# Optimization experiments

Measured on AMD Instinct MI355X. Metric: run time of the kernel, lower is better.

Reference implementation:

```python
import jax, jax.numpy as jnp
import numpy as np

B, S = 64, 128
NQ, C = 2000, 128
K, DE, DC = 64, 64, 64


def _glorot(k, shape):
    lim = float(np.sqrt(6.0 / (shape[0] + shape[1])))
    return jax.random.uniform(k, shape, jnp.float32, -lim, lim)


def setup_inputs() -> dict:
    key = jax.random.key(0)
    ks = jax.random.split(key, 16)
    return {
        'question_seq': jax.random.randint(ks[0], (B, S), 0, NQ, dtype=jnp.int32),
        'correctness_seq': jax.random.randint(ks[1], (B, S), 0, 2, dtype=jnp.int32),
        'q_matrix': (jax.random.uniform(ks[2], (NQ, C)) < 0.15).astype(jnp.float32),
        'E_q': jax.random.normal(ks[3], (NQ, DE), jnp.float32) * 0.02,
        'E_c': jax.random.normal(ks[4], (2, DC), jnp.float32) * 0.02,
        'h0': _glorot(ks[5], (C, K)),
        'W1': _glorot(ks[6], (DC + DE, K)), 'b1': jnp.zeros((K,), jnp.float32),
        'W2': _glorot(ks[7], (3 * K, K)), 'b2': jnp.zeros((K,), jnp.float32),
        'W3': _glorot(ks[8], (3 * K, K)), 'b3': jnp.zeros((K,), jnp.float32),
        'W4': _glorot(ks[9], (2 * K, K)), 'b4': jnp.zeros((K,), jnp.float32),
        'Wab': _glorot(ks[10], (K, 1)), 'bab': jnp.zeros((1,), jnp.float32),
        'Wdiff': _glorot(ks[11], (DE, C)), 'bdiff': jnp.zeros((C,), jnp.float32),
        'Wdisc': _glorot(ks[12], (DE, 1)), 'bdisc': jnp.zeros((1,), jnp.float32),
    }


def _forward(question_seq, correctness_seq, q_matrix, E_q, E_c, h0,
             W1, b1, W2, b2, W3, b3, W4, b4,
             Wab, bab, Wdiff, bdiff, Wdisc, bdisc):
    e_emb = E_q[question_seq]                 # [B,S,DE]
    c_emb = E_c[correctness_seq]              # [B,S,DC]
    all_learning = jnp.concatenate([e_emb, c_emb], -1) @ W1 + b1  # [B,S,K]
    q_seq = q_matrix[question_seq]            # [B,S,C]

    h_pre0 = jnp.broadcast_to(h0, (B, C, K))
    h_tilde0 = jnp.einsum('bc,ck->bk', q_seq[:, 0], h0)
    learning0 = jnp.zeros((B, K), jnp.float32)

    xs = (
        jnp.moveaxis(q_seq[:, :-1], 1, 0),        # q_e        [S-1,B,C]
        jnp.moveaxis(all_learning[:, :-1], 1, 0),  # learning   [S-1,B,K]
        jnp.moveaxis(q_seq[:, 1:], 1, 0),         # q_next     [S-1,B,C]
        jnp.moveaxis(e_emb[:, 1:], 1, 0),         # e_next     [S-1,B,DE]
    )

    def step(carry, x):
        h_pre, h_tilde_pre, learning_pre = carry
        q_e, learning, q_next, e_next = x
        cat = jnp.concatenate([learning_pre, learning, h_tilde_pre], -1)  # [B,3K]
        learning_gain = jnp.tanh(cat @ W2 + b2)
        gamma_l = jax.nn.sigmoid(cat @ W3 + b3)
        LG = gamma_l * (learning_gain + 1.0) * 0.5                       # [B,K]
        LG_tilde = q_e[:, :, None] * LG[:, None, :]                      # [B,C,K] rank-1 scatter
        gate_in = jnp.concatenate(
            [h_pre, jnp.broadcast_to(LG[:, None, :], (B, C, K))], -1)    # [B,C,2K]
        gamma_f = jax.nn.sigmoid(gate_in @ W4 + b4)
        h = LG_tilde + gamma_f * h_pre                                   # [B,C,K]
        ability = jax.nn.sigmoid(jnp.squeeze(h @ Wab + bab, -1)) * q_next  # [B,C]
        diff = jax.nn.sigmoid(e_next @ Wdiff + bdiff) * q_next             # [B,C]
        disc = jax.nn.sigmoid(e_next @ Wdisc + bdisc) * 5.0                # [B,1]
        y = jax.nn.sigmoid(jnp.sum(disc * (ability - diff), -1))          # [B]
        h_tilde = jnp.einsum('bc,bck->bk', q_next, h)
        return (h, h_tilde, learning), y

    _, ys = jax.lax.scan(step, (h_pre0, h_tilde0, learning0), xs)  # ys [S-1,B]
    pred = jnp.concatenate([jnp.zeros((B, 1), jnp.float32), ys.T], axis=1)  # [B,S]
    return pred


def reference(question_seq, correctness_seq, q_matrix, E_q, E_c, h0,
              W1, b1, W2, b2, W3, b3, W4, b4,
              Wab, bab, Wdiff, bdiff, Wdisc, bdisc):
    return _forward(question_seq, correctness_seq, q_matrix, E_q, E_c, h0,
                    W1, b1, W2, b2, W3, b3, W4, b4,
                    Wab, bab, Wdiff, bdiff, Wdisc, bdisc)
```

## Files before the change

kernel.cpp:

```cpp
#include <hip/hip_runtime.h>


constexpr int BB = 64, SS = 128, CD = 128;
constexpr int RECF = 136;
constexpr int HP2  = 72;

typedef short bf16x8 __attribute__((ext_vector_type(8)));
typedef float f32x4  __attribute__((ext_vector_type(4)));

#define BAR() asm volatile("s_waitcnt lgkmcnt(0)\ns_barrier" ::: "memory")

__device__ __forceinline__ short f2bf(float x) {
  unsigned u = __builtin_bit_cast(unsigned, x);
  unsigned r = u + 0x7fffu + ((u >> 16) & 1u);
  return (short)(r >> 16);
}
__device__ __forceinline__ unsigned pk2bf(float a, float b) {
  unsigned ua = __builtin_bit_cast(unsigned, a);
  unsigned ub = __builtin_bit_cast(unsigned, b);
  unsigned ra = ua + 0x7fffu + ((ua >> 16) & 1u);
  unsigned rb = ub + 0x7fffu + ((ub >> 16) & 1u);
  return (ra >> 16) | (rb & 0xffff0000u);
}
__device__ __forceinline__ float sigm(float x) {
  return __builtin_amdgcn_rcpf(1.f + __expf(-x));
}
__device__ __forceinline__ bf16x8 pack8(float4 a, float4 b) {
  uint4 u = {pk2bf(a.x, a.y), pk2bf(a.z, a.w), pk2bf(b.x, b.y), pk2bf(b.z, b.w)};
  return __builtin_bit_cast(bf16x8, u);
}
__device__ __forceinline__ void store_bf4(short* p, float a, float b, float c, float d) {
  uint2 v = {pk2bf(a, b), pk2bf(c, d)};
  *(uint2*)p = v;
}

__global__ void pcK(const float* __restrict__ W1, const float* __restrict__ W2,
                    const float* __restrict__ W3, const float* __restrict__ Ec,
                    const float* __restrict__ b1,
                    float* __restrict__ Kws, float* __restrict__ Uws) {
  int m = blockIdx.x, tid = threadIdx.x;
  if (m < 4) {
    const float* src = (m < 2 ? W2 : W3) + (m & 1) * 64 * 64;
    int k = tid & 63, dg = tid >> 6;
    float acc[16];
    #pragma unroll
    for (int i = 0; i < 16; ++i) acc[i] = 0.f;
    for (int j = 0; j < 64; ++j) {
      float w = src[j * 64 + k];
      #pragma unroll
      for (int i = 0; i < 16; ++i) acc[i] += W1[(dg * 16 + i) * 64 + j] * w;
    }
    #pragma unroll
    for (int i = 0; i < 16; ++i) Kws[m * 4096 + (dg * 16 + i) * 64 + k] = acc[i];
  } else {
    __shared__ float alc[2][64];
    if (tid < 128) {
      int cr = tid >> 6, k = tid & 63;
      float s = b1[k];
      for (int d = 0; d < 64; ++d) s += Ec[cr * 64 + d] * W1[(64 + d) * 64 + k];
      alc[cr][k] = s;
    }
    __syncthreads();
    if (tid < 128) {
      int cr = tid >> 6, k = tid & 63;
      float u2a = 0.f, u2b = 0.f, u3a = 0.f, u3b = 0.f;
      for (int j = 0; j < 64; ++j) {
        float a = alc[cr][j];
        u2a += a * W2[j * 64 + k];       u2b += a * W2[(64 + j) * 64 + k];
        u3a += a * W3[j * 64 + k];       u3b += a * W3[(64 + j) * 64 + k];
      }
      Uws[(0 + cr) * 64 + k] = u2a;  Uws[(2 + cr) * 64 + k] = u2b;
      Uws[(4 + cr) * 64 + k] = u3a;  Uws[(6 + cr) * 64 + k] = u3b;
    }
  }
}

__global__ void pcT(const float* __restrict__ Eq, const float* __restrict__ qmat,
                    const float* __restrict__ Wdiff, const float* __restrict__ bdiff,
                    const float* __restrict__ Wdisc, const float* __restrict__ bdisc,
                    const float* __restrict__ Kws,
                    float* __restrict__ T, float* __restrict__ DIFF, float* __restrict__ DISCq) {
  int q0 = blockIdx.x * 8, tid = threadIdx.x;
  __shared__ float e[8][64];
  for (int i = tid; i < 512; i += 256) e[i >> 6][i & 63] = Eq[(q0 + (i >> 6)) * 64 + (i & 63)];
  __syncthreads();
  {
    int m = tid >> 6, k = tid & 63;
    float acc[8] = {0.f, 0.f, 0.f, 0.f, 0.f, 0.f, 0.f, 0.f};
    for (int d = 0; d < 64; ++d) {
      float w = Kws[m * 4096 + d * 64 + k];
      #pragma unroll
      for (int qq = 0; qq < 8; ++qq) acc[qq] += e[qq][d] * w;
    }
    #pragma unroll
    for (int qq = 0; qq < 8; ++qq) T[(q0 + qq) * 256 + m * 64 + k] = acc[qq];
  }
  if (tid < 128) {
    int c = tid;
    float acc[8] = {0.f, 0.f, 0.f, 0.f, 0.f, 0.f, 0.f, 0.f};
    for (int d = 0; d < 64; ++d) {
      float w = Wdiff[d * 128 + c];
      #pragma unroll
      for (int qq = 0; qq < 8; ++qq) acc[qq] += e[qq][d] * w;
    }
    #pragma unroll
    for (int qq = 0; qq < 8; ++qq)
      DIFF[(q0 + qq) * 128 + c] = qmat[(q0 + qq) * 128 + c] * sigm(acc[qq] + bdiff[c]);
  } else if (tid < 136) {
    int qq = tid - 128;
    float s = 0.f;
    for (int d = 0; d < 64; ++d) s += e[qq][d] * Wdisc[d];
    DISCq[q0 + qq] = 5.f * sigm(s + bdisc[0]);
  }
}

__global__ void pcR(const int* __restrict__ qs, const int* __restrict__ cs,
                    const float* __restrict__ qmat,
                    const float* __restrict__ b2, const float* __restrict__ b3,
                    const float* __restrict__ T, const float* __restrict__ Uws,
                    float* __restrict__ REC) {
  int tid = threadIdx.x;
  for (int i = 0; i < 4; ++i) {
    int bs = blockIdx.x * 4 + i;
    int t  = bs & (SS - 1);
    int q_t = qs[bs];
    float* rec = REC + (size_t)bs * RECF;
    if (tid < 64) {
      int k = tid;
      float v2 = b2[k], v3 = b3[k];
      if (t >= 1) {
        int q1 = qs[bs - 1], c1 = cs[bs - 1];
        v2 += T[q1 * 256 + 64 + k]  + Uws[(2 + c1) * 64 + k];
        v3 += T[q1 * 256 + 192 + k] + Uws[(6 + c1) * 64 + k];
      }
      if (t >= 2) {
        int q2 = qs[bs - 2], c2 = cs[bs - 2];
        v2 += T[q2 * 256 + k]       + Uws[(0 + c2) * 64 + k];
        v3 += T[q2 * 256 + 128 + k] + Uws[(4 + c2) * 64 + k];
      }
      int pp = (k & 15) * 4 + (k >> 4);
      rec[pp] = v2; rec[64 + pp] = v3;
    }
    unsigned long long m = __ballot(qmat[q_t * 128 + tid] > 0.5f);
    int wv = tid >> 6, lane = tid & 63;
    if (lane == 0) {
      rec[128 + wv * 2]     = __uint_as_float((unsigned)m);
      rec[128 + wv * 2 + 1] = __uint_as_float((unsigned)(m >> 32));
    }
  }
}

__global__ void pcY(const int* __restrict__ qs, const float* __restrict__ qmat,
                    const float* __restrict__ DIFF, const float* __restrict__ DISCq,
                    const float* __restrict__ YP, const float* __restrict__ bab,
                    float* __restrict__ out) {
  int tid = threadIdx.x, lane = tid & 63, wv = tid >> 6;
  const float bab0 = bab[0];
  __shared__ float red[4][2];
  #pragma unroll
  for (int i = 0; i < 4; ++i) {
    int bs = blockIdx.x * 4 + i;
    int t  = bs & (SS - 1);
    float v = 0.f;
    if (t != 0) {
      int q_t = qs[bs];
      float yp = YP[(size_t)bs * 128 + tid];
      float qn = qmat[q_t * 128 + tid] > 0.5f ? 1.f : 0.f;
      v = sigm(yp + bab0) * qn - DIFF[q_t * 128 + tid];
    }
    v += __shfl_xor(v, 32); v += __shfl_xor(v, 16); v += __shfl_xor(v, 8);
    v += __shfl_xor(v, 4);  v += __shfl_xor(v, 2);  v += __shfl_xor(v, 1);
    if (lane == 0) red[i][wv] = v;
  }
  __syncthreads();
  if (tid < 4) {
    int bs = blockIdx.x * 4 + tid;
    int t  = bs & (SS - 1);
    if (t == 0) out[bs] = 0.f;
    else        out[bs] = sigm(DISCq[qs[bs]] * (red[tid][0] + red[tid][1]));
  }
}

__global__ __launch_bounds__(256, 1) __attribute__((amdgpu_waves_per_eu(1, 1)))
void lpkt_main(
    const float* __restrict__ h0,
    const float* __restrict__ W2, const float* __restrict__ W3,
    const float* __restrict__ W4, const float* __restrict__ b4,
    const float* __restrict__ Wab,
    const float* __restrict__ REC, float* __restrict__ YP) {
  __shared__ __align__(16) short hsb[CD * HP2];
  __shared__ __align__(16) short lgb[4 * 64];
  __shared__ __align__(16) float htbuf[3][64];

  const int b    = blockIdx.x;
  const int tid  = threadIdx.x;
  const int lane = tid & 63;
  const int wv   = tid >> 6;
  const int col  = lane & 15;
  const int quad = lane >> 4;
  const int bS   = b * SS;
  const f32x4 zz = {0.f, 0.f, 0.f, 0.f};

  const float* W4a = W4;
  const float* W4b = W4 + 64 * 64;
  const float* W2c = W2 + 128 * 64;
  const float* W3c = W3 + 128 * 64;

  bf16x8 bw4[4][2], bwb[4][2], bw2[4][2], bw3[4][2], bwab[2];
  float b4r[4];
  #pragma unroll
  for (int nb = 0; nb < 4; ++nb) {
    #pragma unroll
    for (int half = 0; half < 2; ++half)
      #pragma unroll
      for (int j = 0; j < 8; ++j) {
        int p  = half * 32 + quad * 8 + j;
        int ke = (p & 3) * 16 + (p >> 2);
        int kk = ke * 64 + nb * 16 + col;
        bw4[nb][half][j] = f2bf(W4a[kk]);
        bwb[nb][half][j] = f2bf(W4b[kk]);
        bw2[nb][half][j] = f2bf(W2c[kk]);
        bw3[nb][half][j] = f2bf(W3c[kk]);
      }
    b4r[nb] = b4[nb * 16 + col];
  }
  #pragma unroll
  for (int half = 0; half < 2; ++half)
    #pragma unroll
    for (int j = 0; j < 8; ++j) {
      int p  = half * 32 + quad * 8 + j;
      int ke = (p & 3) * 16 + (p >> 2);
      bwab[half][j] = (col == 0) ? f2bf(Wab[ke]) : (short)0;
    }

  float h2[2][4][4];
  #pragma unroll
  for (int mt = 0; mt < 2; ++mt)
    #pragma unroll
    for (int reg = 0; reg < 4; ++reg) {
      int c = 32 * wv + 16 * mt + 4 * quad + reg;
      #pragma unroll
      for (int n = 0; n < 4; ++n) h2[mt][reg][n] = h0[c * 64 + n * 16 + col];
      store_bf4(&hsb[c * HP2 + col * 4],
                h2[mt][reg][0], h2[mt][reg][1], h2[mt][reg][2], h2[mt][reg][3]);
    }
  if (tid < 192) htbuf[tid >> 6][tid & 63] = 0.f;
  __syncthreads();

  float qeR[2][4];
  {
    unsigned qw = __float_as_uint(REC[(size_t)bS * RECF + 128 + wv]);
    float pk[4] = {0.f, 0.f, 0.f, 0.f};
    #pragma unroll
    for (int mt = 0; mt < 2; ++mt) {
      #pragma unroll
      for (int reg = 0; reg < 4; ++reg)
        qeR[mt][reg] = (float)((qw >> (16 * mt + 4 * quad + reg)) & 1u);
      #pragma unroll
      for (int n = 0; n < 4; ++n)
        pk[n] += qeR[mt][0] * h2[mt][0][n] + qeR[mt][1] * h2[mt][1][n]
               + qeR[mt][2] * h2[mt][2][n] + qeR[mt][3] * h2[mt][3][n];
    }
    #pragma unroll
    for (int n = 0; n < 4; ++n) {
      pk[n] += __shfl_xor(pk[n], 16);
      pk[n] += __shfl_xor(pk[n], 32);
    }
    if (quad == 0) {
      #pragma unroll
      for (int n = 0; n < 4; ++n) atomicAdd(&htbuf[1][col * 4 + n], pk[n]);
    }
  }

  unsigned qbw[2];
  qbw[1] = __float_as_uint(REC[(size_t)(bS + 1) * RECF + 128 + wv]);
  qbw[0] = __float_as_uint(REC[(size_t)(bS + 2) * RECF + 128 + wv]);
  float4 pb2[2], pb3[2];
  pb2[1] = *(const float4*)&REC[(size_t)(bS + 1) * RECF + col * 4];
  pb3[1] = *(const float4*)&REC[(size_t)(bS + 1) * RECF + 64 + col * 4];
  pb2[0] = *(const float4*)&REC[(size_t)(bS + 2) * RECF + col * 4];
  pb3[0] = *(const float4*)&REC[(size_t)(bS + 2) * RECF + 64 + col * 4];
  BAR();

  float qnR[2][4];

  for (int t = 1; t < SS; ++t) {
    const float* htb = htbuf[t % 3];
    float4 x0 = *(const float4*)&htb[quad * 8];
    float4 x1 = *(const float4*)&htb[quad * 8 + 4];
    float4 x2 = *(const float4*)&htb[32 + quad * 8];
    float4 x3 = *(const float4*)&htb[32 + quad * 8 + 4];
    bf16x8 af[2][2];
    #pragma unroll
    for (int mt = 0; mt < 2; ++mt) {
      int r = 32 * wv + 16 * mt + col;
      af[mt][0] = *(const bf16x8*)&hsb[r * HP2 + quad * 8];
      af[mt][1] = *(const bf16x8*)&hsb[r * HP2 + 32 + quad * 8];
    }

    unsigned qw = qbw[t & 1];
    #pragma unroll
    for (int mt = 0; mt < 2; ++mt)
      #pragma unroll
      for (int reg = 0; reg < 4; ++reg)
        qnR[mt][reg] = (float)((qw >> (16 * mt + 4 * quad + reg)) & 1u);
    float4 base2 = pb2[t & 1], base3 = pb3[t & 1];
    {
      int tn = (t + 2 < SS) ? t + 2 : SS - 1;
      const float* rn = REC + (size_t)(bS + tn) * RECF;
      qbw[t & 1] = __float_as_uint(rn[128 + wv]);
      pb2[t & 1] = *(const float4*)&rn[col * 4];
      pb3[t & 1] = *(const float4*)&rn[64 + col * 4];
    }

    f32x4 acc[2][4];
    #pragma unroll
    for (int mt = 0; mt < 2; ++mt)
      #pragma unroll
      for (int nb = 0; nb < 4; ++nb) {
        acc[mt][nb] = __builtin_amdgcn_mfma_f32_16x16x32_bf16(af[mt][0], bw4[nb][0], zz, 0, 0, 0);
        acc[mt][nb] = __builtin_amdgcn_mfma_f32_16x16x32_bf16(af[mt][1], bw4[nb][1], acc[mt][nb], 0, 0, 0);
      }
    #pragma unroll
    for (int mt = 0; mt < 2; ++mt) {
      f32x4 ya = __builtin_amdgcn_mfma_f32_16x16x32_bf16(af[mt][0], bwab[0], zz, 0, 0, 0);
      ya = __builtin_amdgcn_mfma_f32_16x16x32_bf16(af[mt][1], bwab[1], ya, 0, 0, 0);
      if (col == 0)
        *(float4*)&YP[((size_t)bS + t - 1) * 128 + 32 * wv + 16 * mt + 4 * quad]
            = make_float4(ya[0], ya[1], ya[2], ya[3]);
    }

    bf16x8 hf0 = pack8(x0, x1), hf1 = pack8(x2, x3);
    float lg[4];
    #pragma unroll
    for (int nb = 0; nb < 4; ++nb) {
      f32x4 a2 = __builtin_amdgcn_mfma_f32_16x16x32_bf16(hf0, bw2[nb][0], zz, 0, 0, 0);
      a2 = __builtin_amdgcn_mfma_f32_16x16x32_bf16(hf1, bw2[nb][1], a2, 0, 0, 0);
      f32x4 a3 = __builtin_amdgcn_mfma_f32_16x16x32_bf16(hf0, bw3[nb][0], zz, 0, 0, 0);
      a3 = __builtin_amdgcn_mfma_f32_16x16x32_bf16(hf1, bw3[nb][1], a3, 0, 0, 0);
      float u2 = a2[0] + ((const float*)&base2)[nb];
      float u3 = a3[0] + ((const float*)&base3)[nb];
      lg[nb] = sigm(u3) * sigm(2.f * u2);
    }
    if (quad == 0) store_bf4(&lgb[wv * 64 + col * 4], lg[0], lg[1], lg[2], lg[3]);
    bf16x8 lf0 = *(const bf16x8*)&lgb[wv * 64 + quad * 8];
    bf16x8 lf1 = *(const bf16x8*)&lgb[wv * 64 + 32 + quad * 8];
    float tvv[4];
    #pragma unroll
    for (int nb = 0; nb < 4; ++nb) {
      f32x4 bb = __builtin_amdgcn_mfma_f32_16x16x32_bf16(lf0, bwb[nb][0], zz, 0, 0, 0);
      bb = __builtin_amdgcn_mfma_f32_16x16x32_bf16(lf1, bwb[nb][1], bb, 0, 0, 0);
      tvv[nb] = bb[0] + b4r[nb];
    }

    #pragma unroll
    for (int mt = 0; mt < 2; ++mt)
      #pragma unroll
      for (int reg = 0; reg < 4; ++reg) {
        int c = 32 * wv + 16 * mt + 4 * quad + reg;
        #pragma unroll
        for (int nb = 0; nb < 4; ++nb) {
          float g = sigm(acc[mt][nb][reg] + tvv[nb]);
          h2[mt][reg][nb] = qeR[mt][reg] * lg[nb] + g * h2[mt][reg][nb];
        }
        store_bf4(&hsb[c * HP2 + col * 4],
                  h2[mt][reg][0], h2[mt][reg][1], h2[mt][reg][2], h2[mt][reg][3]);
      }

    {
      float pk[4] = {0.f, 0.f, 0.f, 0.f};
      #pragma unroll
      for (int mt = 0; mt < 2; ++mt)
        #pragma unroll
        for (int nb = 0; nb < 4; ++nb)
          pk[nb] += qnR[mt][0] * h2[mt][0][nb] + qnR[mt][1] * h2[mt][1][nb]
                  + qnR[mt][2] * h2[mt][2][nb] + qnR[mt][3] * h2[mt][3][nb];
      #pragma unroll
      for (int nb = 0; nb < 4; ++nb) {
        pk[nb] += __shfl_xor(pk[nb], 16);
        pk[nb] += __shfl_xor(pk[nb], 32);
      }
      if (quad == 0) {
        float* dst = htbuf[(t + 1) % 3];
        #pragma unroll
        for (int nb = 0; nb < 4; ++nb) atomicAdd(&dst[col * 4 + nb], pk[nb]);
      }
    }
    if (wv == 3) htbuf[(t + 2) % 3][lane] = 0.f;
    #pragma unroll
    for (int mt = 0; mt < 2; ++mt)
      #pragma unroll
      for (int reg = 0; reg < 4; ++reg) qeR[mt][reg] = qnR[mt][reg];
    BAR();
  }

  #pragma unroll
  for (int mt = 0; mt < 2; ++mt) {
    int r = 32 * wv + 16 * mt + col;
    bf16x8 af0 = *(const bf16x8*)&hsb[r * HP2 + quad * 8];
    bf16x8 af1 = *(const bf16x8*)&hsb[r * HP2 + 32 + quad * 8];
    f32x4 ya = __builtin_amdgcn_mfma_f32_16x16x32_bf16(af0, bwab[0], zz, 0, 0, 0);
    ya = __builtin_amdgcn_mfma_f32_16x16x32_bf16(af1, bwab[1], ya, 0, 0, 0);
    if (col == 0)
      *(float4*)&YP[((size_t)bS + 127) * 128 + 32 * wv + 16 * mt + 4 * quad]
          = make_float4(ya[0], ya[1], ya[2], ya[3]);
  }
}

extern "C" void kernel_launch(void* const* d_in, const int* in_sizes, int n_in,
                              void* d_out, int out_size, void* d_ws, size_t ws_size,
                              hipStream_t stream) {
  const int*   qs    = (const int*)d_in[0];
  const int*   cs    = (const int*)d_in[1];
  const float* qmat  = (const float*)d_in[2];
  const float* Eq    = (const float*)d_in[3];
  const float* Ec    = (const float*)d_in[4];
  const float* h0    = (const float*)d_in[5];
  const float* W1    = (const float*)d_in[6];
  const float* b1    = (const float*)d_in[7];
  const float* W2    = (const float*)d_in[8];
  const float* b2    = (const float*)d_in[9];
  const float* W3    = (const float*)d_in[10];
  const float* b3    = (const float*)d_in[11];
  const float* W4    = (const float*)d_in[12];
  const float* b4    = (const float*)d_in[13];
  const float* Wab   = (const float*)d_in[14];
  const float* bab   = (const float*)d_in[15];
  const float* Wdiff = (const float*)d_in[16];
  const float* bdiff = (const float*)d_in[17];
  const float* Wdisc = (const float*)d_in[18];
  const float* bdisc = (const float*)d_in[19];
  float* out = (float*)d_out;

  float* w = (float*)d_ws;
  float* Kws   = w;
  float* Uws   = Kws + 16384;
  float* T     = Uws + 512;
  float* DIFF  = T + 512000;
  float* DISCq = DIFF + 256000;
  float* REC   = DISCq + 2000;
  float* YP    = REC + (size_t)BB * SS * RECF;

  pcK<<<5, 256, 0, stream>>>(W1, W2, W3, Ec, b1, Kws, Uws);
  pcT<<<250, 256, 0, stream>>>(Eq, qmat, Wdiff, bdiff, Wdisc, bdisc, Kws, T, DIFF, DISCq);
  pcR<<<BB * SS / 4, 128, 0, stream>>>(qs, cs, qmat, b2, b3, T, Uws, REC);
  lpkt_main<<<BB, 256, 0, stream>>>(h0, W2, W3, W4, b4, Wab, REC, YP);
  pcY<<<BB * SS / 4, 128, 0, stream>>>(qs, qmat, DIFF, DISCq, YP, bab, out);
}
```

Measured before the change: 429.5 us.

## Process two batch sequences per block to interleave independent recurrences

Each workgroup of the recurrent scan now handles two batch rows instead of one, and the grid is halved from 64 to 32 blocks. The two independent recurrences are interleaved within each timestep so their MFMA chains and LDS traffic can hide each other's latency, and the per-step barrier cost is shared by both. In exchange each block does twice the serial work, register pressure roughly doubles, and only 32 of the GPU's compute units are occupied.

```diff
diff --git a/kernel.cpp b/kernel.cpp
--- a/kernel.cpp
+++ b/kernel.cpp
@@ -188,17 +188,18 @@
     const float* __restrict__ W4, const float* __restrict__ b4,
     const float* __restrict__ Wab,
     const float* __restrict__ REC, float* __restrict__ YP) {
-  __shared__ __align__(16) short hsb[CD * HP2];
-  __shared__ __align__(16) short lgb[4 * 64];
-  __shared__ __align__(16) float htbuf[3][64];
-
-  const int b    = blockIdx.x;
+  __shared__ __align__(16) short hsb[2][CD * HP2];
+  __shared__ __align__(16) short lgb[2][4 * 64];
+  __shared__ __align__(16) float htbuf[2][3][64];
+
+  const int blk  = blockIdx.x;
   const int tid  = threadIdx.x;
   const int lane = tid & 63;
   const int wv   = tid >> 6;
   const int col  = lane & 15;
   const int quad = lane >> 4;
-  const int bS   = b * SS;
+  const int bS0  = (blk * 2) * SS;
+  const int bS1  = (blk * 2 + 1) * SS;
   const f32x4 zz = {0.f, 0.f, 0.f, 0.f};
 
   const float* W4a = W4;
@@ -233,33 +234,40 @@
       bwab[half][j] = (col == 0) ? f2bf(Wab[ke]) : (short)0;
     }
 
-  float h2[2][4][4];
+  float h2[2][2][4][4];
   #pragma unroll
   for (int mt = 0; mt < 2; ++mt)
     #pragma unroll
     for (int reg = 0; reg < 4; ++reg) {
       int c = 32 * wv + 16 * mt + 4 * quad + reg;
       #pragma unroll
-      for (int n = 0; n < 4; ++n) h2[mt][reg][n] = h0[c * 64 + n * 16 + col];
-      store_bf4(&hsb[c * HP2 + col * 4],
-                h2[mt][reg][0], h2[mt][reg][1], h2[mt][reg][2], h2[mt][reg][3]);
-    }
-  if (tid < 192) htbuf[tid >> 6][tid & 63] = 0.f;
+      for (int n = 0; n < 4; ++n) {
+        float v = h0[c * 64 + n * 16 + col];
+        h2[0][mt][reg][n] = v; h2[1][mt][reg][n] = v;
+      }
+      store_bf4(&hsb[0][c * HP2 + col * 4],
+                h2[0][mt][reg][0], h2[0][mt][reg][1], h2[0][mt][reg][2], h2[0][mt][reg][3]);
+      store_bf4(&hsb[1][c * HP2 + col * 4],
+                h2[0][mt][reg][0], h2[0][mt][reg][1], h2[0][mt][reg][2], h2[0][mt][reg][3]);
+    }
+  for (int i = tid; i < 384; i += 256) ((float*)htbuf)[i] = 0.f;
   __syncthreads();
 
-  float qeR[2][4];
-  {
+  float qeR[2][2][4];
+  #pragma unroll
+  for (int bt = 0; bt < 2; ++bt) {
+    int bS = bt ? bS1 : bS0;
     unsigned qw = __float_as_uint(REC[(size_t)bS * RECF + 128 + wv]);
     float pk[4] = {0.f, 0.f, 0.f, 0.f};
     #pragma unroll
     for (int mt = 0; mt < 2; ++mt) {
       #pragma unroll
       for (int reg = 0; reg < 4; ++reg)
-        qeR[mt][reg] = (float)((qw >> (16 * mt + 4 * quad + reg)) & 1u);
+        qeR[bt][mt][reg] = (float)((qw >> (16 * mt + 4 * quad + reg)) & 1u);
       #pragma unroll
       for (int n = 0; n < 4; ++n)
-        pk[n] += qeR[mt][0] * h2[mt][0][n] + qeR[mt][1] * h2[mt][1][n]
-               + qeR[mt][2] * h2[mt][2][n] + qeR[mt][3] * h2[mt][3][n];
+        pk[n] += qeR[bt][mt][0] * h2[bt][mt][0][n] + qeR[bt][mt][1] * h2[bt][mt][1][n]
+               + qeR[bt][mt][2] * h2[bt][mt][2][n] + qeR[bt][mt][3] * h2[bt][mt][3][n];
     }
     #pragma unroll
     for (int n = 0; n < 4; ++n) {
@@ -268,142 +276,170 @@
     }
     if (quad == 0) {
       #pragma unroll
-      for (int n = 0; n < 4; ++n) atomicAdd(&htbuf[1][col * 4 + n], pk[n]);
-    }
-  }
-
-  unsigned qbw[2];
-  qbw[1] = __float_as_uint(REC[(size_t)(bS + 1) * RECF + 128 + wv]);
-  qbw[0] = __float_as_uint(REC[(size_t)(bS + 2) * RECF + 128 + wv]);
-  float4 pb2[2], pb3[2];
-  pb2[1] = *(const float4*)&REC[(size_t)(bS + 1) * RECF + col * 4];
-  pb3[1] = *(const float4*)&REC[(size_t)(bS + 1) * RECF + 64 + col * 4];
-  pb2[0] = *(const float4*)&REC[(size_t)(bS + 2) * RECF + col * 4];
-  pb3[0] = *(const float4*)&REC[(size_t)(bS + 2) * RECF + 64 + col * 4];
+      for (int n = 0; n < 4; ++n) atomicAdd(&htbuf[bt][1][col * 4 + n], pk[n]);
+    }
+  }
+
+  unsigned qbw[2][2];
+  float4 pb2[2][2], pb3[2][2];
+  #pragma unroll
+  for (int bt = 0; bt < 2; ++bt) {
+    int bS = bt ? bS1 : bS0;
+    qbw[bt][1] = __float_as_uint(REC[(size_t)(bS + 1) * RECF + 128 + wv]);
+    qbw[bt][0] = __float_as_uint(REC[(size_t)(bS + 2) * RECF + 128 + wv]);
+    pb2[bt][1] = *(const float4*)&REC[(size_t)(bS + 1) * RECF + col * 4];
+    pb3[bt][1] = *(const float4*)&REC[(size_t)(bS + 1) * RECF + 64 + col * 4];
+    pb2[bt][0] = *(const float4*)&REC[(size_t)(bS + 2) * RECF + col * 4];
+    pb3[bt][0] = *(const float4*)&REC[(size_t)(bS + 2) * RECF + 64 + col * 4];
+  }
   BAR();
 
-  float qnR[2][4];
+  float qnR[2][2][4];
 
   for (int t = 1; t < SS; ++t) {
-    const float* htb = htbuf[t % 3];
-    float4 x0 = *(const float4*)&htb[quad * 8];
-    float4 x1 = *(const float4*)&htb[quad * 8 + 4];
-    float4 x2 = *(const float4*)&htb[32 + quad * 8];
-    float4 x3 = *(const float4*)&htb[32 + quad * 8 + 4];
-    bf16x8 af[2][2];
-    #pragma unroll
-    for (int mt = 0; mt < 2; ++mt) {
-      int r = 32 * wv + 16 * mt + col;
-      af[mt][0] = *(const bf16x8*)&hsb[r * HP2 + quad * 8];
-      af[mt][1] = *(const bf16x8*)&hsb[r * HP2 + 32 + quad * 8];
-    }
-
-    unsigned qw = qbw[t & 1];
-    #pragma unroll
-    for (int mt = 0; mt < 2; ++mt)
-      #pragma unroll
-      for (int reg = 0; reg < 4; ++reg)
-        qnR[mt][reg] = (float)((qw >> (16 * mt + 4 * quad + reg)) & 1u);
-    float4 base2 = pb2[t & 1], base3 = pb3[t & 1];
-    {
+    float4 x0[2], x1[2], x2[2], x3[2];
+    bf16x8 af[2][2][2];
+    #pragma unroll
+    for (int bt = 0; bt < 2; ++bt) {
+      const float* htb = htbuf[bt][t % 3];
+      x0[bt] = *(const float4*)&htb[quad * 8];
+      x1[bt] = *(const float4*)&htb[quad * 8 + 4];
+      x2[bt] = *(const float4*)&htb[32 + quad * 8];
+      x3[bt] = *(const float4*)&htb[32 + quad * 8 + 4];
+      #pragma unroll
+      for (int mt = 0; mt < 2; ++mt) {
+        int r = 32 * wv + 16 * mt + col;
+        af[bt][mt][0] = *(const bf16x8*)&hsb[bt][r * HP2 + quad * 8];
+        af[bt][mt][1] = *(const bf16x8*)&hsb[bt][r * HP2 + 32 + quad * 8];
+      }
+    }
+
+    float4 base2[2], base3[2];
+    #pragma unroll
+    for (int bt = 0; bt < 2; ++bt) {
+      int bS = bt ? bS1 : bS0;
+      unsigned qw = qbw[bt][t & 1];
+      #pragma unroll
+      for (int mt = 0; mt < 2; ++mt)
+        #pragma unroll
+        for (int reg = 0; reg < 4; ++reg)
+          qnR[bt][mt][reg] = (float)((qw >> (16 * mt + 4 * quad + reg)) & 1u);
+      base2[bt] = pb2[bt][t & 1]; base3[bt] = pb3[bt][t & 1];
       int tn = (t + 2 < SS) ? t + 2 : SS - 1;
       const float* rn = REC + (size_t)(bS + tn) * RECF;
-      qbw[t & 1] = __float_as_uint(rn[128 + wv]);
-      pb2[t & 1] = *(const float4*)&rn[col * 4];
-      pb3[t & 1] = *(const float4*)&rn[64 + col * 4];
-    }
-
-    f32x4 acc[2][4];
-    #pragma unroll
-    for (int mt = 0; mt < 2; ++mt)
+      qbw[bt][t & 1] = __float_as_uint(rn[128 + wv]);
+      pb2[bt][t & 1] = *(const float4*)&rn[col * 4];
+      pb3[bt][t & 1] = *(const float4*)&rn[64 + col * 4];
+    }
+
+    f32x4 acc[2][2][4];
+    #pragma unroll
+    for (int bt = 0; bt < 2; ++bt)
+      #pragma unroll
+      for (int mt = 0; mt < 2; ++mt)
+        #pragma unroll
+        for (int nb = 0; nb < 4; ++nb) {
+          acc[bt][mt][nb] = __builtin_amdgcn_mfma_f32_16x16x32_bf16(af[bt][mt][0], bw4[nb][0], zz, 0, 0, 0);
+          acc[bt][mt][nb] = __builtin_amdgcn_mfma_f32_16x16x32_bf16(af[bt][mt][1], bw4[nb][1], acc[bt][mt][nb], 0, 0, 0);
+        }
+    #pragma unroll
+    for (int bt = 0; bt < 2; ++bt) {
+      int bS = bt ? bS1 : bS0;
+      #pragma unroll
+      for (int mt = 0; mt < 2; ++mt) {
+        f32x4 ya = __builtin_amdgcn_mfma_f32_16x16x32_bf16(af[bt][mt][0], bwab[0], zz, 0, 0, 0);
+        ya = __builtin_amdgcn_mfma_f32_16x16x32_bf16(af[bt][mt][1], bwab[1], ya, 0, 0, 0);
+        if (col == 0)
+          *(float4*)&YP[((size_t)bS + t - 1) * 128 + 32 * wv + 16 * mt + 4 * quad]
+              = make_float4(ya[0], ya[1], ya[2], ya[3]);
+      }
+    }
+
+    float lg[2][4], tvv[2][4];
+    #pragma unroll
+    for (int bt = 0; bt < 2; ++bt) {
+      bf16x8 hf0 = pack8(x0[bt], x1[bt]), hf1 = pack8(x2[bt], x3[bt]);
       #pragma unroll
       for (int nb = 0; nb < 4; ++nb) {
-        acc[mt][nb] = __builtin_amdgcn_mfma_f32_16x16x32_bf16(af[mt][0], bw4[nb][0], zz, 0, 0, 0);
-        acc[mt][nb] = __builtin_amdgcn_mfma_f32_16x16x32_bf16(af[mt][1], bw4[nb][1], acc[mt][nb], 0, 0, 0);
-      }
-    #pragma unroll
-    for (int mt = 0; mt < 2; ++mt) {
-      f32x4 ya = __builtin_amdgcn_mfma_f32_16x16x32_bf16(af[mt][0], bwab[0], zz, 0, 0, 0);
-      ya = __builtin_amdgcn_mfma_f32_16x16x32_bf16(af[mt][1], bwab[1], ya, 0, 0, 0);
-      if (col == 0)
-        *(float4*)&YP[((size_t)bS + t - 1) * 128 + 32 * wv + 16 * mt + 4 * quad]
-            = make_float4(ya[0], ya[1], ya[2], ya[3]);
-    }
-
-    bf16x8 hf0 = pack8(x0, x1), hf1 = pack8(x2, x3);
-    float lg[4];
-    #pragma unroll
-    for (int nb = 0; nb < 4; ++nb) {
-      f32x4 a2 = __builtin_amdgcn_mfma_f32_16x16x32_bf16(hf0, bw2[nb][0], zz, 0, 0, 0);
-      a2 = __builtin_amdgcn_mfma_f32_16x16x32_bf16(hf1, bw2[nb][1], a2, 0, 0, 0);
-      f32x4 a3 = __builtin_amdgcn_mfma_f32_16x16x32_bf16(hf0, bw3[nb][0], zz, 0, 0, 0);
-      a3 = __builtin_amdgcn_mfma_f32_16x16x32_bf16(hf1, bw3[nb][1], a3, 0, 0, 0);
-      float u2 = a2[0] + ((const float*)&base2)[nb];
-      float u3 = a3[0] + ((const float*)&base3)[nb];
-      lg[nb] = sigm(u3) * sigm(2.f * u2);
-    }
-    if (quad == 0) store_bf4(&lgb[wv * 64 + col * 4], lg[0], lg[1], lg[2], lg[3]);
-    bf16x8 lf0 = *(const bf16x8*)&lgb[wv * 64 + quad * 8];
-    bf16x8 lf1 = *(const bf16x8*)&lgb[wv * 64 + 32 + quad * 8];
-    float tvv[4];
-    #pragma unroll
-    for (int nb = 0; nb < 4; ++nb) {
-      f32x4 bb = __builtin_amdgcn_mfma_f32_16x16x32_bf16(lf0, bwb[nb][0], zz, 0, 0, 0);
-      bb = __builtin_amdgcn_mfma_f32_16x16x32_bf16(lf1, bwb[nb][1], bb, 0, 0, 0);
-      tvv[nb] = bb[0] + b4r[nb];
-    }
-
-    #pragma unroll
-    for (int mt = 0; mt < 2; ++mt)
-      #pragma unroll
-      for (int reg = 0; reg < 4; ++reg) {
-        int c = 32 * wv + 16 * mt + 4 * quad + reg;
-        #pragma unroll
-        for (int nb = 0; nb < 4; ++nb) {
-          float g = sigm(acc[mt][nb][reg] + tvv[nb]);
-          h2[mt][reg][nb] = qeR[mt][reg] * lg[nb] + g * h2[mt][reg][nb];
+        f32x4 a2 = __builtin_amdgcn_mfma_f32_16x16x32_bf16(hf0, bw2[nb][0], zz, 0, 0, 0);
+        a2 = __builtin_amdgcn_mfma_f32_16x16x32_bf16(hf1, bw2[nb][1], a2, 0, 0, 0);
+        f32x4 a3 = __builtin_amdgcn_mfma_f32_16x16x32_bf16(hf0, bw3[nb][0], zz, 0, 0, 0);
+        a3 = __builtin_amdgcn_mfma_f32_16x16x32_bf16(hf1, bw3[nb][1], a3, 0, 0, 0);
+        float u2 = a2[0] + ((const float*)&base2[bt])[nb];
+        float u3 = a3[0] + ((const float*)&base3[bt])[nb];
+        lg[bt][nb] = sigm(u3) * sigm(2.f * u2);
+      }
+      if (quad == 0)
+        store_bf4(&lgb[bt][wv * 64 + col * 4], lg[bt][0], lg[bt][1], lg[bt][2], lg[bt][3]);
+    }
+    #pragma unroll
+    for (int bt = 0; bt < 2; ++bt) {
+      bf16x8 lf0 = *(const bf16x8*)&lgb[bt][wv * 64 + quad * 8];
+      bf16x8 lf1 = *(const bf16x8*)&lgb[bt][wv * 64 + 32 + quad * 8];
+      #pragma unroll
+      for (int nb = 0; nb < 4; ++nb) {
+        f32x4 bb = __builtin_amdgcn_mfma_f32_16x16x32_bf16(lf0, bwb[nb][0], zz, 0, 0, 0);
+        bb = __builtin_amdgcn_mfma_f32_16x16x32_bf16(lf1, bwb[nb][1], bb, 0, 0, 0);
+        tvv[bt][nb] = bb[0] + b4r[nb];
+      }
+    }
+
+    #pragma unroll
+    for (int bt = 0; bt < 2; ++bt) {
+      #pragma unroll
+      for (int mt = 0; mt < 2; ++mt)
+        #pragma unroll
+        for (int reg = 0; reg < 4; ++reg) {
+          int c = 32 * wv + 16 * mt + 4 * quad + reg;
+          #pragma unroll
+          for (int nb = 0; nb < 4; ++nb) {
+            float g = sigm(acc[bt][mt][nb][reg] + tvv[bt][nb]);
+            h2[bt][mt][reg][nb] = qeR[bt][mt][reg] * lg[bt][nb] + g * h2[bt][mt][reg][nb];
+          }
+          store_bf4(&hsb[bt][c * HP2 + col * 4],
+                    h2[bt][mt][reg][0], h2[bt][mt][reg][1], h2[bt][mt][reg][2], h2[bt][mt][reg][3]);
         }
-        store_bf4(&hsb[c * HP2 + col * 4],
-                  h2[mt][reg][0], h2[mt][reg][1], h2[mt][reg][2], h2[mt][reg][3]);
-      }
-
-    {
       float pk[4] = {0.f, 0.f, 0.f, 0.f};
       #pragma unroll
       for (int mt = 0; mt < 2; ++mt)
         #pragma unroll
         for (int nb = 0; nb < 4; ++nb)
-          pk[nb] += qnR[mt][0] * h2[mt][0][nb] + qnR[mt][1] * h2[mt][1][nb]
-                  + qnR[mt][2] * h2[mt][2][nb] + qnR[mt][3] * h2[mt][3][nb];
+          pk[nb] += qnR[bt][mt][0] * h2[bt][mt][0][nb] + qnR[bt][mt][1] * h2[bt][mt][1][nb]
+                  + qnR[bt][mt][2] * h2[bt][mt][2][nb] + qnR[bt][mt][3] * h2[bt][mt][3][nb];
       #pragma unroll
       for (int nb = 0; nb < 4; ++nb) {
         pk[nb] += __shfl_xor(pk[nb], 16);
         pk[nb] += __shfl_xor(pk[nb], 32);
       }
       if (quad == 0) {
-        float* dst = htbuf[(t + 1) % 3];
+        float* dst = htbuf[bt][(t + 1) % 3];
         #pragma unroll
         for (int nb = 0; nb < 4; ++nb) atomicAdd(&dst[col * 4 + nb], pk[nb]);
       }
-    }
-    if (wv == 3) htbuf[(t + 2) % 3][lane] = 0.f;
-    #pragma unroll
-    for (int mt = 0; mt < 2; ++mt)
-      #pragma unroll
-      for (int reg = 0; reg < 4; ++reg) qeR[mt][reg] = qnR[mt][reg];
+      #pragma unroll
+      for (int mt = 0; mt < 2; ++mt)
+        #pragma unroll
+        for (int reg = 0; reg < 4; ++reg) qeR[bt][mt][reg] = qnR[bt][mt][reg];
+    }
+    if (wv == 2) htbuf[0][(t + 2) % 3][lane] = 0.f;
+    if (wv == 3) htbuf[1][(t + 2) % 3][lane] = 0.f;
     BAR();
   }
 
   #pragma unroll
-  for (int mt = 0; mt < 2; ++mt) {
-    int r = 32 * wv + 16 * mt + col;
-    bf16x8 af0 = *(const bf16x8*)&hsb[r * HP2 + quad * 8];
-    bf16x8 af1 = *(const bf16x8*)&hsb[r * HP2 + 32 + quad * 8];
-    f32x4 ya = __builtin_amdgcn_mfma_f32_16x16x32_bf16(af0, bwab[0], zz, 0, 0, 0);
-    ya = __builtin_amdgcn_mfma_f32_16x16x32_bf16(af1, bwab[1], ya, 0, 0, 0);
-    if (col == 0)
-      *(float4*)&YP[((size_t)bS + 127) * 128 + 32 * wv + 16 * mt + 4 * quad]
-          = make_float4(ya[0], ya[1], ya[2], ya[3]);
+  for (int bt = 0; bt < 2; ++bt) {
+    int bS = bt ? bS1 : bS0;
+    #pragma unroll
+    for (int mt = 0; mt < 2; ++mt) {
+      int r = 32 * wv + 16 * mt + col;
+      bf16x8 af0 = *(const bf16x8*)&hsb[bt][r * HP2 + quad * 8];
+      bf16x8 af1 = *(const bf16x8*)&hsb[bt][r * HP2 + 32 + quad * 8];
+      f32x4 ya = __builtin_amdgcn_mfma_f32_16x16x32_bf16(af0, bwab[0], zz, 0, 0, 0);
+      ya = __builtin_amdgcn_mfma_f32_16x16x32_bf16(af1, bwab[1], ya, 0, 0, 0);
+      if (col == 0)
+        *(float4*)&YP[((size_t)bS + 127) * 128 + 32 * wv + 16 * mt + 4 * quad]
+            = make_float4(ya[0], ya[1], ya[2], ya[3]);
+    }
   }
 }
 
@@ -444,6 +480,6 @@
   pcK<<<5, 256, 0, stream>>>(W1, W2, W3, Ec, b1, Kws, Uws);
   pcT<<<250, 256, 0, stream>>>(Eq, qmat, Wdiff, bdiff, Wdisc, bdisc, Kws, T, DIFF, DISCq);
   pcR<<<BB * SS / 4, 128, 0, stream>>>(qs, cs, qmat, b2, b3, T, Uws, REC);
-  lpkt_main<<<BB, 256, 0, stream>>>(h0, W2, W3, W4, b4, Wab, REC, YP);
+  lpkt_main<<<BB / 2, 256, 0, stream>>>(h0, W2, W3, W4, b4, Wab, REC, YP);
   pcY<<<BB * SS / 4, 128, 0, stream>>>(qs, qmat, DIFF, DISCq, YP, bab, out);
 }
```

Measured after the change: 835.4 us. 1.95x slower.
